# Performance work log

Hardware: AMD Instinct MI355X
Metric: run time of the kernel (lower is better)

## Reference

```python
import jax, jax.numpy as jnp
import numpy as np

B, T, D = 1, 2048, 2048
N_HEADS, N_KV = 32, 8
HD = D // N_HEADS          # 64
G = N_HEADS // N_KV        # 4 query heads per kv head


def setup_inputs() -> dict:
    key = jax.random.key(0)
    ks = jax.random.split(key, 8)
    x = jax.random.normal(ks[0], (B, T, D), dtype=jnp.float32)
    cos = jax.random.uniform(ks[1], (1, 1, T, HD), dtype=jnp.float32)
    sin = jax.random.uniform(ks[2], (1, 1, T, HD), dtype=jnp.float32)
    attention_mask = jnp.ones((B, T), dtype=jnp.int32)
    s = 1.0 / np.sqrt(D)
    Wq = jax.random.normal(ks[3], (D, D), dtype=jnp.float32) * s
    Wk = jax.random.normal(ks[4], (D, N_KV * HD), dtype=jnp.float32) * s
    Wv = jax.random.normal(ks[5], (D, N_KV * HD), dtype=jnp.float32) * s
    Wo = jax.random.normal(ks[6], (D, D), dtype=jnp.float32) * s
    return {"x": x, "cos": cos, "sin": sin, "attention_mask": attention_mask,
            "Wq": Wq, "Wk": Wk, "Wv": Wv, "Wo": Wo}


def rotate_half(t):
    t1, t2 = jnp.split(t, 2, axis=-1)
    return jnp.concatenate((-t2, t1), axis=-1)


def reference(x, cos, sin, attention_mask, Wq, Wk, Wv, Wo):
    b, t, d = x.shape
    # projections (Linear, no bias); weights stored as [in, out]
    q = (x @ Wq).reshape(b, t, N_HEADS, HD).transpose(0, 2, 1, 3)   # [B,H,T,hd]
    k = (x @ Wk).reshape(b, t, N_KV, HD).transpose(0, 2, 1, 3)      # [B,Kv,T,hd]
    v = (x @ Wv).reshape(b, t, N_KV, HD).transpose(0, 2, 1, 3)      # [B,Kv,T,hd]
    # RoPE
    q = q * cos + rotate_half(q) * sin
    k = k * cos + rotate_half(k) * sin
    # GQA without materializing repeated KV: group query heads by kv head
    qg = q.reshape(b, N_KV, G, t, HD)                               # [B,Kv,G,T,hd]
    scale = 1.0 / jnp.sqrt(jnp.asarray(HD, dtype=x.dtype))
    scores = jnp.einsum('bkgqd,bkcd->bkgqc', qg, k) * scale          # [B,Kv,G,T,T]
    neg = jnp.finfo(x.dtype).min
    # padding mask: (1 - mask) * finfo.min, broadcast over heads/query pos
    pad = (1.0 - attention_mask.astype(x.dtype)) * neg               # [B,T]
    scores = scores + pad[:, None, None, None, :]
    # causal mask
    causal = jnp.tril(jnp.ones((t, t), dtype=bool))
    scores = jnp.where(causal[None, None, None, :, :], scores, neg)
    p = jax.nn.softmax(scores, axis=-1)
    y = jnp.einsum('bkgqc,bkcd->bkgqd', p, v)                        # [B,Kv,G,T,hd]
    y = y.reshape(b, N_HEADS, t, HD).transpose(0, 2, 1, 3).reshape(b, t, d)
    return y @ Wo
```

## Files before the change

### kernel.cpp

```cpp
#include <hip/hip_runtime.h>
#include <hip/hip_bf16.h>
#include <math.h>

typedef __attribute__((ext_vector_type(4))) float f32x4;
typedef __attribute__((ext_vector_type(8))) short bf16x8;
typedef __attribute__((ext_vector_type(4))) short bf16x4;
typedef unsigned short u16;
typedef unsigned int u32;


__device__ __forceinline__ float exp2fast(float x) {
    return __builtin_amdgcn_exp2f(x);
}
__device__ __forceinline__ u16 f2bf(float f) {
    return __builtin_bit_cast(u16, __float2bfloat16(f));
}
__device__ __forceinline__ float bf2f(u16 h) {
    return __builtin_bit_cast(float, ((u32)h) << 16);
}

#define GLL16(gsrc, ldst) __builtin_amdgcn_global_load_lds( \
    (const __attribute__((address_space(1))) u32*)(gsrc),   \
    (__attribute__((address_space(3))) u32*)(ldst), 16, 0, 0)

__device__ __forceinline__ void tconv_body(const float* __restrict__ in, u16* __restrict__ out,
                                           int R, int C, int bx, int by,
                                           float (*tile)[33], int tx, int ty) {
    int c0 = bx * 32, r0 = by * 32;
    #pragma unroll
    for (int i = 0; i < 4; ++i)
        tile[ty + i * 8][tx] = in[(size_t)(r0 + ty + i * 8) * C + c0 + tx];
    __syncthreads();
    #pragma unroll
    for (int i = 0; i < 4; ++i)
        out[(size_t)(c0 + ty + i * 8) * R + r0 + tx] = f2bf(tile[tx][ty + i * 8]);
}

__global__ void k_prep(const float* __restrict__ x, u16* __restrict__ xb,
                       const float* __restrict__ Wq, const float* __restrict__ Wk,
                       const float* __restrict__ Wv, const float* __restrict__ Wo,
                       u16* __restrict__ Wt, u16* __restrict__ WoT) {
    __shared__ float tile[32][33];
    const int r = blockIdx.x;
    const int tx = threadIdx.x, ty = threadIdx.y;
    if (r < 4096) {
        int tid = ty * 32 + tx;
        int base = (r * 256 + tid) * 4;
        float4 v = *(const float4*)(x + base);
        ushort4 o;
        o.x = f2bf(v.x); o.y = f2bf(v.y); o.z = f2bf(v.z); o.w = f2bf(v.w);
        *(ushort4*)(xb + base) = o;
    } else if (r < 8192) {
        int rr = r - 4096;  tconv_body(Wq, Wt, 2048, 2048, rr & 63, rr >> 6, tile, tx, ty);
    } else if (r < 9216) {
        int rr = r - 8192;  tconv_body(Wk, Wt + (size_t)2048 * 2048, 2048, 512, rr & 15, rr >> 4, tile, tx, ty);
    } else if (r < 10240) {
        int rr = r - 9216;  tconv_body(Wv, Wt + (size_t)2560 * 2048, 2048, 512, rr & 15, rr >> 4, tile, tx, ty);
    } else {
        int rr = r - 10240; tconv_body(Wo, WoT, 2048, 2048, rr & 63, rr >> 6, tile, tx, ty);
    }
}

__global__ void k_ropekv(u16* QKV,
                         const float* __restrict__ cosp, const float* __restrict__ sinp,
                         const int* __restrict__ maskp, float* __restrict__ padf,
                         u16* __restrict__ Vt, int* __restrict__ padAny) {
    __shared__ u16 tile[32][34];
    const int r = blockIdx.x;
    const int tx = threadIdx.x, ty = threadIdx.y;
    if (r < 2048) {
        int t = r;
        int tid = ty * 32 + tx;
        if (tid == 0)
            padf[t] = maskp[t] ? 0.0f : -3.4028235e38f;
        int hh = tid >> 5, j = tid & 31;
        u16* base = QKV + (size_t)t * 3072 + 2048 + hh * 64;
        float q1 = bf2f(base[j]);
        float q2 = bf2f(base[j + 32]);
        float c1 = cosp[t * 64 + j],      s1 = sinp[t * 64 + j];
        float c2 = cosp[t * 64 + j + 32], s2 = sinp[t * 64 + j + 32];
        base[j]      = f2bf(q1 * c1 - q2 * s1);
        base[j + 32] = f2bf(q2 * c2 + q1 * s2);
    } else if (r < 3072) {
        int rr = r - 2048;
        int c0 = (rr & 15) * 32, r0 = (rr >> 4) * 32;
        const u16* in = QKV + 2560;
        #pragma unroll
        for (int i = 0; i < 4; ++i)
            tile[ty + i * 8][tx] = in[(size_t)(r0 + ty + i * 8) * 3072 + c0 + tx];
        __syncthreads();
        int kv = r0 + tx;
        int kvp = (kv & ~63) + (((kv >> 5) & 1) << 5) + (((kv >> 2) & 3) << 3)
                + (((kv >> 4) & 1) << 2) + (kv & 3);
        #pragma unroll
        for (int i = 0; i < 4; ++i)
            Vt[(size_t)(c0 + ty + i * 8) * 2048 + kvp] = tile[tx][ty + i * 8];
    } else {
        int t64 = r - 3072;
        int tid = ty * 32 + tx;
        if (tid < 64) {
            bool anypad = (maskp[t64 * 64 + tid] == 0);
            unsigned long long b = __ballot(anypad);
            if (tid == 0) padAny[t64] = (b != 0ULL) ? 1 : 0;
        }
    }
}

template<int OUTF32>
__global__ __launch_bounds__(256) void k_gemm(const u16* __restrict__ A, int lda,
                                              const u16* __restrict__ Bt,
                                              void* __restrict__ Cv,
                                              int M, int N, int K) {
    __shared__ u16 As[2][64 * 64];
    __shared__ u16 Bs[2][128 * 64];
    const int tid = threadIdx.x;
    const int w = tid >> 6, lane = tid & 63;
    const int wr = w & 1, wc = w >> 1;
    const int g = lane >> 4, l15 = lane & 15;
    const int m0 = blockIdx.y * 64, n0 = blockIdx.x * 128;

    f32x4 acc[2][4] = {};

    const u16* gA[2];
    const u16* gB[4];
    #pragma unroll
    for (int i = 0; i < 2; ++i) {
        int c = tid + i * 256;
        int rr = c >> 3, kc = (c & 7) ^ (rr & 7);
        gA[i] = A + (size_t)(m0 + rr) * lda + kc * 8;
    }
    #pragma unroll
    for (int i = 0; i < 4; ++i) {
        int c = tid + i * 256;
        int rr = c >> 3, kc = (c & 7) ^ (rr & 7);
        gB[i] = Bt + (size_t)(n0 + rr) * K + kc * 8;
    }

    auto stageAB = [&](int b, int k0) {
        #pragma unroll
        for (int i = 0; i < 2; ++i)
            GLL16(gA[i] + k0, &As[b][(tid + i * 256) * 8]);
        #pragma unroll
        for (int i = 0; i < 4; ++i)
            GLL16(gB[i] + k0, &Bs[b][(tid + i * 256) * 8]);
    };

    stageAB(0, 0);
    __syncthreads();
    int buf = 0;

    for (int k0 = 0; k0 < K; k0 += 64) {
        int kn = k0 + 64;
        if (kn < K) stageAB(buf ^ 1, kn);

        bf16x8 af[2][2], bfr[4][2];
        #pragma unroll
        for (int mt = 0; mt < 2; ++mt) {
            int row = wr * 32 + mt * 16 + l15;
            int rb = row * 64;
            #pragma unroll
            for (int kk = 0; kk < 2; ++kk) {
                int slot = (kk * 4 + g) ^ (row & 7);
                af[mt][kk] = *(const bf16x8*)&As[buf][rb + slot * 8];
            }
        }
        #pragma unroll
        for (int nt = 0; nt < 4; ++nt) {
            int row = wc * 64 + nt * 16 + l15;
            int rb = row * 64;
            #pragma unroll
            for (int kk = 0; kk < 2; ++kk) {
                int slot = (kk * 4 + g) ^ (row & 7);
                bfr[nt][kk] = *(const bf16x8*)&Bs[buf][rb + slot * 8];
            }
        }
        #pragma unroll
        for (int mt = 0; mt < 2; ++mt)
            #pragma unroll
            for (int nt = 0; nt < 4; ++nt) {
                acc[mt][nt] = __builtin_amdgcn_mfma_f32_16x16x32_bf16(af[mt][0], bfr[nt][0], acc[mt][nt], 0, 0, 0);
                acc[mt][nt] = __builtin_amdgcn_mfma_f32_16x16x32_bf16(af[mt][1], bfr[nt][1], acc[mt][nt], 0, 0, 0);
            }
        __syncthreads();
        buf ^= 1;
    }
    #pragma unroll
    for (int mt = 0; mt < 2; ++mt) {
        #pragma unroll
        for (int nt = 0; nt < 4; ++nt) {
            int mrow = m0 + wr * 32 + mt * 16 + g * 4;
            int ncol = n0 + wc * 64 + nt * 16 + l15;
            #pragma unroll
            for (int rr = 0; rr < 4; ++rr) {
                float v = acc[mt][nt][rr];
                if (OUTF32) ((float*)Cv)[(size_t)(mrow + rr) * N + ncol] = v;
                else        ((u16*)Cv)[(size_t)(mrow + rr) * N + ncol] = f2bf(v);
            }
        }
    }
}

__global__ __launch_bounds__(512) void k_attn(const u16* __restrict__ QKV,
                                              const u16* __restrict__ VtG,
                                              const float* __restrict__ cosp,
                                              const float* __restrict__ sinp,
                                              const float* __restrict__ padf,
                                              const int* __restrict__ padAny,
                                              u16* __restrict__ Ob) {
    __shared__ u16 Ks[2][64 * 64];
    __shared__ u16 Vs[2][64 * 64];
    const int kvh = blockIdx.y;
    const int xq = (kvh >= 4) ? (int)blockIdx.x : 63 - (int)blockIdx.x;
    const int tid = threadIdx.x;
    const int w = tid >> 6, lane = tid & 63;
    const int g = lane >> 4, l15 = lane & 15;
    const int h = kvh * 4 + (w & 3);
    const int q0w = xq * 32 + (w >> 2) * 16;
    const int q = q0w + l15;
    const int myfull = q0w >> 6;
    const int iters = ((xq * 32 + 16) >> 6) + 1;
    const bf16x8 ones8 = {(short)0x3F80, (short)0x3F80, (short)0x3F80, (short)0x3F80,
                          (short)0x3F80, (short)0x3F80, (short)0x3F80, (short)0x3F80};

    bf16x8 qf0, qf1;
    {
        const u16* qrow = QKV + (size_t)q * 3072 + h * 64;
        bf16x8 qr0 = *(const bf16x8*)(qrow + g * 8);
        bf16x8 qr1 = *(const bf16x8*)(qrow + 32 + g * 8);
        const float* cb = cosp + (size_t)q * 64 + g * 8;
        const float* sb = sinp + (size_t)q * 64 + g * 8;
        float clo[8], chi[8], slo[8], shi[8];
        *(f32x4*)clo = *(const f32x4*)cb;       *(f32x4*)(clo + 4) = *(const f32x4*)(cb + 4);
        *(f32x4*)chi = *(const f32x4*)(cb + 32); *(f32x4*)(chi + 4) = *(const f32x4*)(cb + 36);
        *(f32x4*)slo = *(const f32x4*)sb;       *(f32x4*)(slo + 4) = *(const f32x4*)(sb + 4);
        *(f32x4*)shi = *(const f32x4*)(sb + 32); *(f32x4*)(shi + 4) = *(const f32x4*)(sb + 36);
        const float SC = 0.18033688f;
        #pragma unroll
        for (int e = 0; e < 8; ++e) {
            float a = bf2f((u16)qr0[e]);
            float b = bf2f((u16)qr1[e]);
            qf0[e] = (short)f2bf((a * clo[e] - b * slo[e]) * SC);
            qf1[e] = (short)f2bf((b * chi[e] + a * shi[e]) * SC);
        }
    }

    f32x4 oacc[4] = {};
    float m_run = -1e30f, l_run = 0.0f;

    auto stage = [&](int b, int kv0) {
        int p = tid;
        int rr = p >> 3, c = p & 7;
        int cs = c ^ (rr & 7);
        GLL16(QKV + (size_t)(kv0 + rr) * 3072 + 2048 + kvh * 64 + cs * 8, &Ks[b][p * 8]);
        GLL16(VtG + (size_t)(kvh * 64 + rr) * 2048 + kv0 + cs * 8, &Vs[b][p * 8]);
    };

    stage(0, 0);
    __syncthreads();
    int buf = 0;

    for (int t = 0; t < iters; ++t) {
        const int kv0 = t * 64;
        if (t + 1 < iters) stage(buf ^ 1, kv0 + 64);

        if (t <= myfull) {
            const bool masked = (t == myfull);

            f32x4 st[4];
            __builtin_amdgcn_s_setprio(1);
            #pragma unroll
            for (int j = 0; j < 4; ++j) {
                int row = j * 16 + l15;
                int rb = row * 64, sw = (row & 7) << 3;
                bf16x8 kf0 = *(const bf16x8*)&Ks[buf][rb + ((g << 3) ^ sw)];
                bf16x8 kf1 = *(const bf16x8*)&Ks[buf][rb + ((32 + (g << 3)) ^ sw)];
                f32x4 z = {};
                st[j] = __builtin_amdgcn_mfma_f32_16x16x32_bf16(kf0, qf0, z, 0, 0, 0);
                st[j] = __builtin_amdgcn_mfma_f32_16x16x32_bf16(kf1, qf1, st[j], 0, 0, 0);
            }
            __builtin_amdgcn_s_setprio(0);

            float s[4][4];
            float tm = -1e30f;
            if (padAny[t]) {
                #pragma unroll
                for (int j = 0; j < 4; ++j) {
                    f32x4 pd = *(const f32x4*)(padf + kv0 + j * 16 + g * 4);
                    #pragma unroll
                    for (int rr = 0; rr < 4; ++rr) s[j][rr] = st[j][rr] + pd[rr];
                }
            } else {
                #pragma unroll
                for (int j = 0; j < 4; ++j)
                    #pragma unroll
                    for (int rr = 0; rr < 4; ++rr) s[j][rr] = st[j][rr];
            }
            if (masked) {
                #pragma unroll
                for (int j = 0; j < 4; ++j)
                    #pragma unroll
                    for (int rr = 0; rr < 4; ++rr) {
                        int kv = kv0 + j * 16 + g * 4 + rr;
                        if (kv > q) s[j][rr] = -INFINITY;
                    }
            }
            #pragma unroll
            for (int j = 0; j < 4; ++j)
                #pragma unroll
                for (int rr = 0; rr < 4; ++rr) tm = fmaxf(tm, s[j][rr]);
            tm = fmaxf(tm, __shfl_xor(tm, 16));
            tm = fmaxf(tm, __shfl_xor(tm, 32));
            if (__any(tm > m_run + 11.5f)) {
                float m_new = fmaxf(m_run, tm);
                float fac = exp2fast(m_run - m_new);
                #pragma unroll
                for (int dt = 0; dt < 4; ++dt) oacc[dt] *= fac;
                l_run *= fac;
                m_run = m_new;
            }
            bf16x4 pb[4];
            #pragma unroll
            for (int j = 0; j < 4; ++j)
                #pragma unroll
                for (int rr = 0; rr < 4; ++rr)
                    pb[j][rr] = (short)f2bf(exp2fast(s[j][rr] - m_run));
            bf16x8 pbp0 = {pb[0][0], pb[0][1], pb[0][2], pb[0][3],
                           pb[1][0], pb[1][1], pb[1][2], pb[1][3]};
            bf16x8 pbp1 = {pb[2][0], pb[2][1], pb[2][2], pb[2][3],
                           pb[3][0], pb[3][1], pb[3][2], pb[3][3]};

            __builtin_amdgcn_s_setprio(1);
            {
                f32x4 la = {};
                la = __builtin_amdgcn_mfma_f32_16x16x32_bf16(ones8, pbp0, la, 0, 0, 0);
                la = __builtin_amdgcn_mfma_f32_16x16x32_bf16(ones8, pbp1, la, 0, 0, 0);
                l_run += la[0];
            }
            #pragma unroll
            for (int dt = 0; dt < 4; ++dt) {
                int row = dt * 16 + l15;
                int rb = row * 64, sw7 = row & 7;
                bf16x8 v0 = *(const bf16x8*)&Vs[buf][rb + ((g ^ sw7) << 3)];
                bf16x8 v1 = *(const bf16x8*)&Vs[buf][rb + (((4 + g) ^ sw7) << 3)];
                oacc[dt] = __builtin_amdgcn_mfma_f32_16x16x32_bf16(v0, pbp0, oacc[dt], 0, 0, 0);
                oacc[dt] = __builtin_amdgcn_mfma_f32_16x16x32_bf16(v1, pbp1, oacc[dt], 0, 0, 0);
            }
            __builtin_amdgcn_s_setprio(0);
        }
        __syncthreads();
        buf ^= 1;
    }

    float il = 1.0f / l_run;
    u16* orow = Ob + (size_t)q * 3072 + h * 64;
    #pragma unroll
    for (int dt = 0; dt < 4; ++dt) {
        ushort4 o;
        o.x = f2bf(oacc[dt][0] * il);
        o.y = f2bf(oacc[dt][1] * il);
        o.z = f2bf(oacc[dt][2] * il);
        o.w = f2bf(oacc[dt][3] * il);
        *(ushort4*)(orow + dt * 16 + g * 4) = o;
    }
}

extern "C" void kernel_launch(void* const* d_in, const int* in_sizes, int n_in,
                              void* d_out, int out_size, void* d_ws, size_t ws_size,
                              hipStream_t stream) {
    const float* x    = (const float*)d_in[0];
    const float* cosp = (const float*)d_in[1];
    const float* sinp = (const float*)d_in[2];
    const int*   mask = (const int*)d_in[3];
    const float* Wq   = (const float*)d_in[4];
    const float* Wk   = (const float*)d_in[5];
    const float* Wv   = (const float*)d_in[6];
    const float* Wo   = (const float*)d_in[7];
    float* out = (float*)d_out;

    char* ws = (char*)d_ws;
    u16* xb  = (u16*)ws; ws += (size_t)2048 * 2048 * 2;
    u16* Wt  = (u16*)ws; ws += (size_t)3072 * 2048 * 2;
    u16* WoT = (u16*)ws; ws += (size_t)2048 * 2048 * 2;
    u16* QKV = (u16*)ws; ws += (size_t)2048 * 3072 * 2;
    u16* Vt  = (u16*)ws; ws += (size_t)512 * 2048 * 2;
    float* padf = (float*)ws; ws += 2048 * 4;
    int* padAny = (int*)ws;

    dim3 tb(32, 8);
    k_prep<<<14336, tb, 0, stream>>>(x, xb, Wq, Wk, Wv, Wo, Wt, WoT);

    k_gemm<0><<<dim3(24, 32), 256, 0, stream>>>(xb, 2048, Wt, QKV, 2048, 3072, 2048);

    k_ropekv<<<3104, tb, 0, stream>>>(QKV, cosp, sinp, mask, padf, Vt, padAny);

    k_attn<<<dim3(64, 8), 512, 0, stream>>>(QKV, Vt, cosp, sinp, padf, padAny, QKV);

    k_gemm<1><<<dim3(16, 32), 256, 0, stream>>>(QKV, 3072, WoT, out, 2048, 2048, 2048);
}
```

Baseline: 129.4 us.

## Widen attention KV tile to 128 and skip fully masked diagonal subtiles

Result: slower. 133.0 us (+2.8%).

```diff
diff --git a/kernel.cpp b/kernel.cpp
--- a/kernel.cpp
+++ b/kernel.cpp
@@ -207,8 +207,8 @@
                                               const float* __restrict__ padf,
                                               const int* __restrict__ padAny,
                                               u16* __restrict__ Ob) {
-    __shared__ u16 Ks[2][64 * 64];
-    __shared__ u16 Vs[2][64 * 64];
+    __shared__ u16 Ks[2][128 * 64];
+    __shared__ u16 Vs[2][64 * 128];
     const int kvh = blockIdx.y;
     const int xq = (kvh >= 4) ? (int)blockIdx.x : 63 - (int)blockIdx.x;
     const int tid = threadIdx.x;
@@ -217,8 +217,9 @@
     const int h = kvh * 4 + (w & 3);
     const int q0w = xq * 32 + (w >> 2) * 16;
     const int q = q0w + l15;
-    const int myfull = q0w >> 6;
-    const int iters = ((xq * 32 + 16) >> 6) + 1;
+    const int myfull = q0w >> 7;
+    const int jmd = ((q0w & 127) >> 4) + 1;
+    const int iters = ((xq * 32 + 16) >> 7) + 1;
     const bf16x8 ones8 = {(short)0x3F80, (short)0x3F80, (short)0x3F80, (short)0x3F80,
                           (short)0x3F80, (short)0x3F80, (short)0x3F80, (short)0x3F80};
 
@@ -248,11 +249,18 @@
     float m_run = -1e30f, l_run = 0.0f;
 
     auto stage = [&](int b, int kv0) {
-        int p = tid;
-        int rr = p >> 3, c = p & 7;
-        int cs = c ^ (rr & 7);
-        GLL16(QKV + (size_t)(kv0 + rr) * 3072 + 2048 + kvh * 64 + cs * 8, &Ks[b][p * 8]);
-        GLL16(VtG + (size_t)(kvh * 64 + rr) * 2048 + kv0 + cs * 8, &Vs[b][p * 8]);
+        #pragma unroll
+        for (int i = 0; i < 2; ++i) {
+            int p = tid + i * 512;
+            int rr = p >> 3, c = p & 7;
+            int cs = c ^ (rr & 7);
+            GLL16(QKV + (size_t)(kv0 + rr) * 3072 + 2048 + kvh * 64 + cs * 8, &Ks[b][p * 8]);
+            int pv = tid + i * 512;
+            int vr = pv >> 4, vc = pv & 15;
+            int vb = vc >> 3, vs = vc & 7;
+            int vcs = vb * 8 + (vs ^ (vr & 7));
+            GLL16(VtG + (size_t)(kvh * 64 + vr) * 2048 + kv0 + vcs * 8, &Vs[b][pv * 8]);
+        }
     };
 
     stage(0, 0);
@@ -260,16 +268,17 @@
     int buf = 0;
 
     for (int t = 0; t < iters; ++t) {
-        const int kv0 = t * 64;
-        if (t + 1 < iters) stage(buf ^ 1, kv0 + 64);
+        const int kv0 = t * 128;
+        if (t + 1 < iters) stage(buf ^ 1, kv0 + 128);
 
         if (t <= myfull) {
             const bool masked = (t == myfull);
-
-            f32x4 st[4];
+            const int jm = masked ? jmd : 8;
+
+            f32x4 st[8];
             __builtin_amdgcn_s_setprio(1);
             #pragma unroll
-            for (int j = 0; j < 4; ++j) {
+            for (int j = 0; j < 8; ++j) if (j < jm) {
                 int row = j * 16 + l15;
                 int rb = row * 64, sw = (row & 7) << 3;
                 bf16x8 kf0 = *(const bf16x8*)&Ks[buf][rb + ((g << 3) ^ sw)];
@@ -280,34 +289,30 @@
             }
             __builtin_amdgcn_s_setprio(0);
 
-            float s[4][4];
             float tm = -1e30f;
-            if (padAny[t]) {
-                #pragma unroll
-                for (int j = 0; j < 4; ++j) {
+            if (padAny[2 * t] | padAny[2 * t + 1]) {
+                #pragma unroll
+                for (int j = 0; j < 8; ++j) if (j < jm) {
                     f32x4 pd = *(const f32x4*)(padf + kv0 + j * 16 + g * 4);
                     #pragma unroll
-                    for (int rr = 0; rr < 4; ++rr) s[j][rr] = st[j][rr] + pd[rr];
+                    for (int rr = 0; rr < 4; ++rr) st[j][rr] += pd[rr];
                 }
-            } else {
-                #pragma unroll
-                for (int j = 0; j < 4; ++j)
-                    #pragma unroll
-                    for (int rr = 0; rr < 4; ++rr) s[j][rr] = st[j][rr];
             }
             if (masked) {
                 #pragma unroll
-                for (int j = 0; j < 4; ++j)
+                for (int j = 0; j < 8; ++j) if (j < jm) {
                     #pragma unroll
                     for (int rr = 0; rr < 4; ++rr) {
                         int kv = kv0 + j * 16 + g * 4 + rr;
-                        if (kv > q) s[j][rr] = -INFINITY;
+                        if (kv > q) st[j][rr] = -INFINITY;
                     }
-            }
-            #pragma unroll
-            for (int j = 0; j < 4; ++j)
-                #pragma unroll
-                for (int rr = 0; rr < 4; ++rr) tm = fmaxf(tm, s[j][rr]);
+                }
+            }
+            #pragma unroll
+            for (int j = 0; j < 8; ++j) if (j < jm) {
+                #pragma unroll
+                for (int rr = 0; rr < 4; ++rr) tm = fmaxf(tm, st[j][rr]);
+            }
             tm = fmaxf(tm, __shfl_xor(tm, 16));
             tm = fmaxf(tm, __shfl_xor(tm, 32));
             if (__any(tm > m_run + 11.5f)) {
@@ -318,32 +323,38 @@
                 l_run *= fac;
                 m_run = m_new;
             }
-            bf16x4 pb[4];
-            #pragma unroll
-            for (int j = 0; j < 4; ++j)
+            bf16x4 pb[8] = {};
+            #pragma unroll
+            for (int j = 0; j < 8; ++j) if (j < jm) {
                 #pragma unroll
                 for (int rr = 0; rr < 4; ++rr)
-                    pb[j][rr] = (short)f2bf(exp2fast(s[j][rr] - m_run));
-            bf16x8 pbp0 = {pb[0][0], pb[0][1], pb[0][2], pb[0][3],
-                           pb[1][0], pb[1][1], pb[1][2], pb[1][3]};
-            bf16x8 pbp1 = {pb[2][0], pb[2][1], pb[2][2], pb[2][3],
-                           pb[3][0], pb[3][1], pb[3][2], pb[3][3]};
+                    pb[j][rr] = (short)f2bf(exp2fast(st[j][rr] - m_run));
+            }
+            bf16x8 pbp[4];
+            #pragma unroll
+            for (int pr = 0; pr < 4; ++pr)
+                pbp[pr] = bf16x8{pb[2 * pr][0], pb[2 * pr][1], pb[2 * pr][2], pb[2 * pr][3],
+                                 pb[2 * pr + 1][0], pb[2 * pr + 1][1], pb[2 * pr + 1][2], pb[2 * pr + 1][3]};
 
             __builtin_amdgcn_s_setprio(1);
             {
                 f32x4 la = {};
-                la = __builtin_amdgcn_mfma_f32_16x16x32_bf16(ones8, pbp0, la, 0, 0, 0);
-                la = __builtin_amdgcn_mfma_f32_16x16x32_bf16(ones8, pbp1, la, 0, 0, 0);
+                #pragma unroll
+                for (int pr = 0; pr < 4; ++pr) if (2 * pr < jm)
+                    la = __builtin_amdgcn_mfma_f32_16x16x32_bf16(ones8, pbp[pr], la, 0, 0, 0);
                 l_run += la[0];
             }
             #pragma unroll
             for (int dt = 0; dt < 4; ++dt) {
                 int row = dt * 16 + l15;
-                int rb = row * 64, sw7 = row & 7;
-                bf16x8 v0 = *(const bf16x8*)&Vs[buf][rb + ((g ^ sw7) << 3)];
-                bf16x8 v1 = *(const bf16x8*)&Vs[buf][rb + (((4 + g) ^ sw7) << 3)];
-                oacc[dt] = __builtin_amdgcn_mfma_f32_16x16x32_bf16(v0, pbp0, oacc[dt], 0, 0, 0);
-                oacc[dt] = __builtin_amdgcn_mfma_f32_16x16x32_bf16(v1, pbp1, oacc[dt], 0, 0, 0);
+                int rb = row * 128, sw7 = row & 7;
+                #pragma unroll
+                for (int pr = 0; pr < 4; ++pr) if (2 * pr < jm) {
+                    int blk = pr >> 1;
+                    int sl  = (pr & 1) ? (4 + g) : g;
+                    bf16x8 v = *(const bf16x8*)&Vs[buf][rb + ((blk * 8 + (sl ^ sw7)) << 3)];
+                    oacc[dt] = __builtin_amdgcn_mfma_f32_16x16x32_bf16(v, pbp[pr], oacc[dt], 0, 0, 0);
+                }
             }
             __builtin_amdgcn_s_setprio(0);
         }
```
